# Performance work log

Measured on AMD Instinct MI355X. Metric: run time of the kernel, lower is better.

## Reference

```python
import jax, jax.numpy as jnp
import numpy as np

D_MODEL = 1024
NHEAD = 16
SPARSITY = 0.9  # keep prob = 1 - sparsity
NEG = -1e30    # stand-in for -inf; avoids NaN on (rare) fully-masked rows
EPS = 1e-5


def _layernorm(x, g, b):
    mu = jnp.mean(x, axis=-1, keepdims=True)
    var = jnp.mean(jnp.square(x - mu), axis=-1, keepdims=True)
    return (x - mu) * jax.lax.rsqrt(var + EPS) * g + b


def setup_inputs() -> dict:
    key = jax.random.key(0)
    ks = jax.random.split(key, 12)
    B, S, D = 2, 2048, D_MODEL
    H = NHEAD
    s = 1.0 / np.sqrt(D)
    inp = {
        "x": jax.random.normal(ks[0], (B, S, D), jnp.float32),
        # torch: torch.rand((B,H,S,S)) > sparsity, resampled each forward
        "mask": jax.random.uniform(ks[1], (B, H, S, S), jnp.float32) > SPARSITY,
        "Wq": jax.random.normal(ks[2], (D, D), jnp.float32) * s,
        "bq": jnp.zeros((D,), jnp.float32),
        "Wk": jax.random.normal(ks[3], (D, D), jnp.float32) * s,
        "bk": jnp.zeros((D,), jnp.float32),
        "Wv": jax.random.normal(ks[4], (D, D), jnp.float32) * s,
        "bv": jnp.zeros((D,), jnp.float32),
        "Wo": jax.random.normal(ks[5], (D, D), jnp.float32) * s,
        "bo": jnp.zeros((D,), jnp.float32),
        "ln1_g": jnp.ones((D,), jnp.float32),
        "ln1_b": jnp.zeros((D,), jnp.float32),
        "ln2_g": jnp.ones((D,), jnp.float32),
        "ln2_b": jnp.zeros((D,), jnp.float32),
        "W1": jax.random.normal(ks[6], (D, 4 * D), jnp.float32) * s,
        "b1f": jnp.zeros((4 * D,), jnp.float32),
        "W2": jax.random.normal(ks[7], (4 * D, D), jnp.float32) * (1.0 / np.sqrt(4 * D)),
        "b2f": jnp.zeros((D,), jnp.float32),
    }
    return inp


def reference(x, mask, Wq, bq, Wk, bk, Wv, bv, Wo, bo,
              ln1_g, ln1_b, ln2_g, ln2_b, W1, b1f, W2, b2f):
    B, S, D = x.shape
    H = NHEAD
    dk = D // H
    # projections -> (B, H, S, dk)
    q = (x @ Wq + bq).reshape(B, S, H, dk).transpose(0, 2, 1, 3)
    k = (x @ Wk + bk).reshape(B, S, H, dk).transpose(0, 2, 1, 3)
    v = (x @ Wv + bv).reshape(B, S, H, dk).transpose(0, 2, 1, 3)
    scores = jnp.einsum('bhqd,bhkd->bhqk', q, k) / np.sqrt(dk)
    scores = jnp.where(mask, scores, NEG)
    attn = jax.nn.softmax(scores, axis=-1)
    ctx = jnp.einsum('bhqk,bhkd->bhqd', attn, v)          # (B,H,S,dk)
    ctx = ctx.transpose(0, 2, 1, 3).reshape(B, S, D)
    attn_out = ctx @ Wo + bo
    x = _layernorm(x + attn_out, ln1_g, ln1_b)
    ff = jax.nn.relu(x @ W1 + b1f) @ W2 + b2f             # eval: dropout off
    return _layernorm(x + ff, ln2_g, ln2_b)
```

## Files before the change

kernel.cpp:

```cpp
#include <hip/hip_runtime.h>
#include <stdint.h>


typedef __attribute__((ext_vector_type(8))) short short8;
typedef __attribute__((ext_vector_type(4))) float f32x4;
typedef __attribute__((ext_vector_type(4))) unsigned short u16x4;

__device__ __forceinline__ unsigned short f2bf(float f) {
    union { float f; unsigned u; } v; v.f = f;
    unsigned r = v.u + 0x7fffu + ((v.u >> 16) & 1u);
    return (unsigned short)(r >> 16);
}

__device__ __forceinline__ void gload16(const void* gsrc, void* ldst) {
    __builtin_amdgcn_global_load_lds(
        (const __attribute__((address_space(1))) void*)gsrc,
        (__attribute__((address_space(3))) void*)ldst,
        16, 0, 0);
}

__device__ __forceinline__ int SWZ(int b) { return b ^ (((b >> 9) & 1) << 5); }

__global__ __launch_bounds__(256) void f32_to_bf16_k(
    const float* __restrict__ in, unsigned short* __restrict__ out, int n4)
{
    int i = blockIdx.x * 256 + threadIdx.x;
    if (i < n4) {
        f32x4 v = *(const f32x4*)&in[(size_t)i * 4];
        u16x4 o = { f2bf(v[0]), f2bf(v[1]), f2bf(v[2]), f2bf(v[3]) };
        *(u16x4*)&out[(size_t)i * 4] = o;
    }
}

__global__ __launch_bounds__(256) void transpose_k(
    const float* __restrict__ W, unsigned short* __restrict__ Wt, int K, int N)
{
    __shared__ float tile[32][33];
    const int n0 = blockIdx.x * 32, k0 = blockIdx.y * 32;
    const int tx = threadIdx.x & 31, ty = threadIdx.x >> 5;
#pragma unroll
    for (int i = 0; i < 32; i += 8)
        tile[ty + i][tx] = W[(size_t)(k0 + ty + i) * N + n0 + tx];
    __syncthreads();
#pragma unroll
    for (int i = 0; i < 32; i += 8)
        Wt[(size_t)(n0 + ty + i) * K + k0 + tx] = f2bf(tile[tx][ty + i]);
}

__global__ __launch_bounds__(256) void vtrans_k(
    const unsigned short* __restrict__ qkv, unsigned short* __restrict__ vt)
{
    __shared__ unsigned short tile[32][34];
    const int s0 = blockIdx.x * 32;
    const int d0 = blockIdx.y * 32;
    const int bh = blockIdx.z, b = bh >> 4, h = bh & 15;
    const int tx = threadIdx.x & 31, ty = threadIdx.x >> 5;
#pragma unroll
    for (int i = 0; i < 32; i += 8)
        tile[ty + i][tx] = qkv[(size_t)(b * 2048 + s0 + ty + i) * 3072 + 2048 + h * 64 + d0 + tx];
    __syncthreads();
#pragma unroll
    for (int i = 0; i < 32; i += 8)
        vt[((size_t)bh * 64 + d0 + ty + i) * 2048 + s0 + tx] = tile[tx][ty + i];
}

__global__ void concat3_k(const float* a, const float* b, const float* c, float* out)
{
    int i = blockIdx.x * 256 + threadIdx.x;
    if (i < 3072) out[i] = (i < 1024) ? a[i] : (i < 2048 ? b[i - 1024] : c[i - 2048]);
}

__global__ __launch_bounds__(1024) void detect_mask_k(
    const unsigned int* __restrict__ m, int* __restrict__ flag)
{
    __shared__ int f1, f2;
    if (threadIdx.x == 0) { f1 = 0; f2 = 0; }
    __syncthreads();
    int l1 = 0, l2 = 0;
    for (int i = threadIdx.x; i < 65536; i += 1024) {
        unsigned v = m[i];
        l1 |= (v > 1u);
        l2 |= (v != 0u && v != 0x3f800000u);
    }
    if (l1) atomicOr(&f1, 1);
    if (l2) atomicOr(&f2, 1);
    __syncthreads();
    if (threadIdx.x == 0) {
        int mode = 0;
        if (f1) mode = f2 ? 1 : 2;
        *flag = mode;
    }
}

__global__ __launch_bounds__(256) void pack_mask_k(
    const void* __restrict__ mask, const int* __restrict__ flag,
    unsigned long long* __restrict__ packed, long long nelem)
{
    const int mode = *flag;
    const long long stride = (long long)gridDim.x * 256;
    long long i = (long long)blockIdx.x * 256 + threadIdx.x;
    if (mode == 0) {
        const int* m = (const int*)mask;
        for (; i < nelem; i += stride) {
            unsigned long long bl = __ballot(m[i] != 0);
            if ((threadIdx.x & 63) == 0) packed[i >> 6] = bl;
        }
    } else if (mode == 1) {
        const unsigned char* m = (const unsigned char*)mask;
        for (; i < nelem; i += stride) {
            unsigned long long bl = __ballot(m[i] != 0);
            if ((threadIdx.x & 63) == 0) packed[i >> 6] = bl;
        }
    } else {
        const float* m = (const float*)mask;
        for (; i < nelem; i += stride) {
            unsigned long long bl = __ballot(m[i] != 0.f);
            if ((threadIdx.x & 63) == 0) packed[i >> 6] = bl;
        }
    }
}

template<int EPI>
__global__ __launch_bounds__(512) void gemm256_bt(
    const unsigned short* __restrict__ A, const unsigned short* __restrict__ Bt,
    const float* __restrict__ bias, void* __restrict__ Cout,
    int M, int N, int K)
{
    __shared__ __align__(16) unsigned short lds[2][2][256 * 64];
    const int t = threadIdx.x;
    const int lane = t & 63;
    const int wid = t >> 6;
    const int l16 = lane & 15, g = lane >> 4;
    const int wr = wid >> 2, wc = wid & 3;

    const int nbx = gridDim.x, nwg = nbx * gridDim.y;
    const int orig = blockIdx.y * nbx + blockIdx.x;
    const int qq = nwg >> 3, rr = nwg & 7;
    const int xcd = orig & 7, idx = orig >> 3;
    const int wg = (xcd < rr) ? (xcd * (qq + 1) + idx)
                              : (rr * (qq + 1) + (xcd - rr) * qq + idx);
    const int bm = (wg / nbx) * 256, bn = (wg % nbx) * 256;

    const int ntiles = K >> 6;
    auto kof = [&](int s) { return (s < ntiles ? s : ntiles - 1) << 6; };

    auto stage_half = [&](const unsigned short* __restrict__ P, int grow0, int k0,
                          int buf, int ab, int half) {
#pragma unroll
        for (int rnd = 0; rnd < 2; ++rnd) {
            const int off = rnd * 8192 + t * 16;
            const int sw  = SWZ(off);
            const int row = off >> 7;
            const int col = (sw & 127) >> 1;
            gload16(&P[(size_t)(grow0 + half * 128 + row) * K + k0 + col],
                    &lds[buf][ab][half * 8192 + (off >> 1)]);
        }
    };

    auto lda = [&](int buf, int m, int kc) -> short8 {
        const int byte = ((m * 32 + wr * 16 + l16) * 64 + kc * 32 + g * 8) * 2;
        return *(const short8*)((const char*)&lds[buf][0][0] + SWZ(byte));
    };
    auto ldb = [&](int buf, int n, int kc) -> short8 {
        const int byte = ((n * 64 + wc * 16 + l16) * 64 + kc * 32 + g * 8) * 2;
        return *(const short8*)((const char*)&lds[buf][1][0] + SWZ(byte));
    };

    f32x4 acc[8][4] = {};
    short8 af[4][2];

    stage_half(A,  bm, 0,  0, 0, 0);
    stage_half(A,  bm, 0,  0, 0, 1);
    stage_half(Bt, bn, 0,  0, 1, 0);
    stage_half(Bt, bn, 0,  0, 1, 1);
    stage_half(A,  bm, 64, 1, 0, 0);
    stage_half(Bt, bn, 64, 1, 1, 0);
    asm volatile("s_waitcnt vmcnt(4)" ::: "memory");
    __builtin_amdgcn_s_barrier();

#define PH(buf, mh, nh, doLoadA, STAGE_STMT, doVM)                                  \
  {                                                                                  \
    if (doLoadA) {                                                                   \
      _Pragma("unroll") for (int mm = 0; mm < 4; ++mm)                               \
      _Pragma("unroll") for (int kc = 0; kc < 2; ++kc)                               \
        af[mm][kc] = lda(buf, (mh) * 4 + mm, kc);                                    \
    }                                                                                \
    short8 bf[2][2];                                                                 \
    _Pragma("unroll") for (int nn = 0; nn < 2; ++nn)                                 \
    _Pragma("unroll") for (int kc = 0; kc < 2; ++kc)                                 \
      bf[nn][kc] = ldb(buf, (nh) * 2 + nn, kc);                                      \
    STAGE_STMT;                                                                      \
    __builtin_amdgcn_s_barrier();                                                    \
    __builtin_amdgcn_s_setprio(1);                                                   \
    _Pragma("unroll") for (int mm = 0; mm < 4; ++mm)                                 \
    _Pragma("unroll") for (int nn = 0; nn < 2; ++nn)                                 \
    _Pragma("unroll") for (int kc = 0; kc < 2; ++kc)                                 \
      acc[(mh) * 4 + mm][(nh) * 2 + nn] = __builtin_amdgcn_mfma_f32_16x16x32_bf16(   \
          af[mm][kc], bf[nn][kc], acc[(mh) * 4 + mm][(nh) * 2 + nn], 0, 0, 0);       \
    __builtin_amdgcn_s_setprio(0);                                                   \
    if (doVM) { asm volatile("s_waitcnt vmcnt(4)" ::: "memory"); }                   \
    __builtin_amdgcn_s_barrier();                                                    \
  }

    const int half_ntiles = ntiles >> 1;
    for (int i = 0; i < half_ntiles; ++i) {
        const int k1 = (2 * i + 1) << 6;
        const int k2 = kof(2 * i + 2);
        const int k3 = kof(2 * i + 3);
        PH(0, 0, 0, 1, (stage_half(A,  bm, k1, 1, 0, 1)), 0)
        PH(0, 0, 1, 0, (stage_half(Bt, bn, k1, 1, 1, 1)), 0)
        PH(0, 1, 0, 1, (stage_half(A,  bm, k2, 0, 0, 0)), 0)
        PH(0, 1, 1, 0, (stage_half(Bt, bn, k2, 0, 1, 0)), 1)
        PH(1, 0, 0, 1, (stage_half(A,  bm, k2, 0, 0, 1)), 0)
        PH(1, 0, 1, 0, (stage_half(Bt, bn, k2, 0, 1, 1)), 0)
        PH(1, 1, 0, 1, (stage_half(A,  bm, k3, 1, 0, 0)), 0)
        PH(1, 1, 1, 0, (stage_half(Bt, bn, k3, 1, 1, 0)), 1)
    }
#undef PH

#pragma unroll
    for (int m = 0; m < 8; ++m) {
        const int row0 = bm + m * 32 + wr * 16 + g * 4;
#pragma unroll
        for (int n = 0; n < 4; ++n) {
            const int col = bn + n * 64 + wc * 16 + l16;
            const float bb = bias[col];
#pragma unroll
            for (int r = 0; r < 4; ++r) {
                float v = acc[m][n][r] + bb;
                if (EPI == 1) v = fmaxf(v, 0.f);
                ((unsigned short*)Cout)[(size_t)(row0 + r) * N + col] = f2bf(v);
            }
        }
    }
}

template<int EPI>
__global__ __launch_bounds__(256) void gemm_bt(
    const unsigned short* __restrict__ A, const unsigned short* __restrict__ Bt,
    const float* __restrict__ bias, const float* __restrict__ resid,
    void* __restrict__ Cout, int M, int N, int K)
{
    __shared__ unsigned short As[128 * 64];
    __shared__ unsigned short Bs[128 * 64];
    const int t = threadIdx.x;
    const int lane = t & 63, wid = t >> 6;
    const int l16 = lane & 15, g = lane >> 4;
    const int wr = wid >> 1, wc = wid & 1;
    const int bm = blockIdx.y * 128, bn = blockIdx.x * 128;

    f32x4 acc[4][4] = {};

    for (int k0 = 0; k0 < K; k0 += 64) {
        __syncthreads();
#pragma unroll
        for (int i = 0; i < 4; ++i) {
            int linear = i * 2048 + t * 8;
            int row = linear >> 6, col = linear & 63;
            gload16(&A[(size_t)(bm + row) * K + k0 + col], &As[linear]);
        }
#pragma unroll
        for (int i = 0; i < 4; ++i) {
            int linear = i * 2048 + t * 8;
            int row = linear >> 6, col = linear & 63;
            gload16(&Bt[(size_t)(bn + row) * K + k0 + col], &Bs[linear]);
        }
        __syncthreads();
#pragma unroll
        for (int kc = 0; kc < 2; ++kc) {
            short8 a[4], b[4];
#pragma unroll
            for (int m = 0; m < 4; ++m)
                a[m] = *(const short8*)&As[(wr * 64 + m * 16 + l16) * 64 + kc * 32 + g * 8];
#pragma unroll
            for (int n = 0; n < 4; ++n)
                b[n] = *(const short8*)&Bs[(wc * 64 + n * 16 + l16) * 64 + kc * 32 + g * 8];
#pragma unroll
            for (int m = 0; m < 4; ++m)
#pragma unroll
                for (int n = 0; n < 4; ++n)
                    acc[m][n] = __builtin_amdgcn_mfma_f32_16x16x32_bf16(a[m], b[n], acc[m][n], 0, 0, 0);
        }
    }

#pragma unroll
    for (int m = 0; m < 4; ++m) {
        const int row0 = bm + wr * 64 + m * 16 + g * 4;
#pragma unroll
        for (int n = 0; n < 4; ++n) {
            const int col = bn + wc * 64 + n * 16 + l16;
            const float bb = bias[col];
#pragma unroll
            for (int r = 0; r < 4; ++r) {
                float v = acc[m][n][r] + bb;
                const size_t idx = (size_t)(row0 + r) * N + col;
                if (EPI == 2) {
                    ((float*)Cout)[idx] = v + resid[idx];
                } else {
                    if (EPI == 1) v = fmaxf(v, 0.f);
                    ((unsigned short*)Cout)[idx] = f2bf(v);
                }
            }
        }
    }
}

__global__ __launch_bounds__(256) void attn_k(
    const unsigned short* __restrict__ qkv,
    const unsigned short* __restrict__ vt,
    const unsigned long long* __restrict__ pmask,
    unsigned short* __restrict__ ctx)
{
    __shared__ unsigned short Pl[4][16 * 72];
    const int t = threadIdx.x, lane = t & 63, w = t >> 6;
    const int l16 = lane & 15, g = lane >> 4;
    const int bh = blockIdx.y;
    const int b = bh >> 4, h = bh & 15;
    const int q0 = blockIdx.x * 64;

    const size_t rowQ = (size_t)(b * 2048 + q0 + w * 16 + l16) * 3072 + h * 64;
    const short8 qf0 = *(const short8*)&qkv[rowQ + g * 8];
    const short8 qf1 = *(const short8*)&qkv[rowQ + 32 + g * 8];

    const unsigned long long* mbase =
        pmask + ((size_t)bh * 2048 + q0 + w * 16 + g * 4) * 32;
    const unsigned short* vbase = &vt[(size_t)bh * 64 * 2048];

    f32x4 acc[4] = {};
    float lrow[4] = { 0.f, 0.f, 0.f, 0.f };

    for (int kt = 0; kt < 32; ++kt) {
        unsigned long long mw[4];
#pragma unroll
        for (int j = 0; j < 4; ++j) mw[j] = mbase[j * 32 + kt];

        f32x4 s[4] = {};
        __builtin_amdgcn_s_setprio(1);
#pragma unroll
        for (int n = 0; n < 4; ++n) {
            const size_t rowK = (size_t)(b * 2048 + kt * 64 + n * 16 + l16) * 3072 + 1024 + h * 64;
            const short8 kf0 = *(const short8*)&qkv[rowK + g * 8];
            const short8 kf1 = *(const short8*)&qkv[rowK + 32 + g * 8];
            s[n] = __builtin_amdgcn_mfma_f32_16x16x32_bf16(qf0, kf0, s[n], 0, 0, 0);
            s[n] = __builtin_amdgcn_mfma_f32_16x16x32_bf16(qf1, kf1, s[n], 0, 0, 0);
        }
        __builtin_amdgcn_s_setprio(0);

#pragma unroll
        for (int n = 0; n < 4; ++n) {
            const int sh = n * 16 + l16;
#pragma unroll
            for (int j = 0; j < 4; ++j) {
                const bool keep = (mw[j] >> sh) & 1ull;
                const float p = keep ? __expf(s[n][j] * 0.125f) : 0.f;
                s[n][j] = p;
                lrow[j] += p;
            }
        }

#pragma unroll
        for (int n = 0; n < 4; ++n)
#pragma unroll
            for (int j = 0; j < 4; ++j)
                Pl[w][(g * 4 + j) * 72 + n * 16 + l16] = f2bf(s[n][j]);

        __builtin_amdgcn_s_setprio(1);
#pragma unroll
        for (int c = 0; c < 2; ++c) {
            const short8 pf = *(const short8*)&Pl[w][l16 * 72 + c * 32 + g * 8];
#pragma unroll
            for (int n = 0; n < 4; ++n) {
                const short8 vf = *(const short8*)&vbase[(size_t)(n * 16 + l16) * 2048 + kt * 64 + c * 32 + g * 8];
                acc[n] = __builtin_amdgcn_mfma_f32_16x16x32_bf16(pf, vf, acc[n], 0, 0, 0);
            }
        }
        __builtin_amdgcn_s_setprio(0);
    }

#pragma unroll
    for (int j = 0; j < 4; ++j) {
#pragma unroll
        for (int d = 1; d < 16; d <<= 1) lrow[j] += __shfl_xor(lrow[j], d);
        lrow[j] = 1.f / fmaxf(lrow[j], 1e-30f);
    }

#pragma unroll
    for (int n = 0; n < 4; ++n)
#pragma unroll
        for (int j = 0; j < 4; ++j) {
            const int q = q0 + w * 16 + g * 4 + j;
            ctx[(size_t)(b * 2048 + q) * 1024 + h * 64 + n * 16 + l16] = f2bf(acc[n][j] * lrow[j]);
        }
}

template<int WB>
__global__ __launch_bounds__(256) void ln_k(
    const float* __restrict__ in, const float* __restrict__ gw, const float* __restrict__ bw,
    float* __restrict__ outF, unsigned short* __restrict__ outB)
{
    __shared__ float red[2][4];
    const int row = blockIdx.x, t = threadIdx.x;
    const f32x4 v = *(const f32x4*)&in[(size_t)row * 1024 + t * 4];
    float s = v[0] + v[1] + v[2] + v[3];
    float ss = v[0] * v[0] + v[1] * v[1] + v[2] * v[2] + v[3] * v[3];
#pragma unroll
    for (int d = 1; d < 64; d <<= 1) { s += __shfl_xor(s, d); ss += __shfl_xor(ss, d); }
    if ((t & 63) == 0) { red[0][t >> 6] = s; red[1][t >> 6] = ss; }
    __syncthreads();
    s = red[0][0] + red[0][1] + red[0][2] + red[0][3];
    ss = red[1][0] + red[1][1] + red[1][2] + red[1][3];
    const float mu = s * (1.f / 1024.f);
    const float var = ss * (1.f / 1024.f) - mu * mu;
    const float rs = rsqrtf(var + 1e-5f);
    f32x4 y;
#pragma unroll
    for (int e = 0; e < 4; ++e)
        y[e] = (v[e] - mu) * rs * gw[t * 4 + e] + bw[t * 4 + e];
    *(f32x4*)&outF[(size_t)row * 1024 + t * 4] = y;
    if (WB) {
        u16x4 o = { f2bf(y[0]), f2bf(y[1]), f2bf(y[2]), f2bf(y[3]) };
        *(u16x4*)&outB[(size_t)row * 1024 + t * 4] = o;
    }
}

extern "C" void kernel_launch(void* const* d_in, const int* in_sizes, int n_in,
                              void* d_out, int out_size, void* d_ws, size_t ws_size,
                              hipStream_t stream)
{
    (void)n_in; (void)out_size; (void)ws_size;
    const float* x   = (const float*)d_in[0];
    const void*  mask = d_in[1];
    const float* Wq  = (const float*)d_in[2];
    const float* bq  = (const float*)d_in[3];
    const float* Wk  = (const float*)d_in[4];
    const float* bk  = (const float*)d_in[5];
    const float* Wv  = (const float*)d_in[6];
    const float* bv  = (const float*)d_in[7];
    const float* Wo  = (const float*)d_in[8];
    const float* bo  = (const float*)d_in[9];
    const float* g1  = (const float*)d_in[10];
    const float* be1 = (const float*)d_in[11];
    const float* g2  = (const float*)d_in[12];
    const float* be2 = (const float*)d_in[13];
    const float* W1  = (const float*)d_in[14];
    const float* b1  = (const float*)d_in[15];
    const float* W2  = (const float*)d_in[16];
    const float* b2  = (const float*)d_in[17];

    const int M = 4096;
    const long long maskN = in_sizes[1];

    char* wsb = (char*)d_ws;
    size_t off = 0;
    auto alloc = [&](size_t bytes) -> char* {
        char* p = wsb + off;
        off += (bytes + 255) & ~(size_t)255;
        return p;
    };
    int*            flag   = (int*)           alloc(256);
    unsigned long long* pm = (unsigned long long*)alloc((size_t)(maskN / 64) * 8);
    unsigned short* xb     = (unsigned short*)alloc((size_t)M * 1024 * 2);
    unsigned short* wqkvT  = (unsigned short*)alloc((size_t)3072 * 1024 * 2);
    unsigned short* woT    = (unsigned short*)alloc((size_t)1024 * 1024 * 2);
    unsigned short* w1T    = (unsigned short*)alloc((size_t)4096 * 1024 * 2);
    unsigned short* w2T    = (unsigned short*)alloc((size_t)1024 * 4096 * 2);
    float*          bqkv   = (float*)         alloc(3072 * 4);
    unsigned short* qkv    = (unsigned short*)alloc((size_t)M * 3072 * 2);
    unsigned short* vtb    = (unsigned short*)alloc((size_t)32 * 64 * 2048 * 2);
    unsigned short* ctxb   = (unsigned short*)alloc((size_t)M * 1024 * 2);
    float*          r1f    = (float*)         alloc((size_t)M * 1024 * 4);
    float*          x1f    = (float*)         alloc((size_t)M * 1024 * 4);
    unsigned short* x1b    = (unsigned short*)alloc((size_t)M * 1024 * 2);
    unsigned short* hb     = (unsigned short*)alloc((size_t)M * 4096 * 2);

    detect_mask_k<<<1, 1024, 0, stream>>>((const unsigned int*)mask, flag);
    pack_mask_k<<<2048, 256, 0, stream>>>(mask, flag, pm, maskN);
    f32_to_bf16_k<<<4096, 256, 0, stream>>>(x, xb, M * 1024 / 4);
    transpose_k<<<dim3(32, 32),  256, 0, stream>>>(Wq, wqkvT,                1024, 1024);
    transpose_k<<<dim3(32, 32),  256, 0, stream>>>(Wk, wqkvT + 1024 * 1024,  1024, 1024);
    transpose_k<<<dim3(32, 32),  256, 0, stream>>>(Wv, wqkvT + 2048 * 1024,  1024, 1024);
    transpose_k<<<dim3(32, 32),  256, 0, stream>>>(Wo, woT,                  1024, 1024);
    transpose_k<<<dim3(128, 32), 256, 0, stream>>>(W1, w1T, 1024, 4096);
    transpose_k<<<dim3(32, 128), 256, 0, stream>>>(W2, w2T, 4096, 1024);
    concat3_k<<<12, 256, 0, stream>>>(bq, bk, bv, bqkv);

    gemm256_bt<0><<<dim3(12, 16), 512, 0, stream>>>(xb, wqkvT, bqkv, qkv, M, 3072, 1024);
    vtrans_k<<<dim3(64, 2, 32), 256, 0, stream>>>(qkv, vtb);
    attn_k<<<dim3(32, 32), 256, 0, stream>>>(qkv, vtb, pm, ctxb);
    gemm_bt<2><<<dim3(8, 32), 256, 0, stream>>>(ctxb, woT, bo, x, r1f, M, 1024, 1024);
    ln_k<1><<<4096, 256, 0, stream>>>(r1f, g1, be1, x1f, x1b);
    gemm256_bt<1><<<dim3(16, 16), 512, 0, stream>>>(x1b, w1T, b1, hb, M, 4096, 1024);
    gemm_bt<2><<<dim3(8, 32), 256, 0, stream>>>(hb, w2T, b2, x1f, r1f, M, 1024, 4096);
    ln_k<0><<<4096, 256, 0, stream>>>(r1f, g2, be2, (float*)d_out, nullptr);
}
```

Baseline: 1.286 ms.

## Stage K/V tiles in double-buffered swizzled LDS and enlarge attention blocks

The attention kernel now loads each 64-key K tile and V^T tile into LDS with async global-to-LDS loads. It double-buffers them so the next tile's load overlaps the current compute, and uses an XOR swizzle to avoid bank conflicts. Blocks grow to 512 threads covering 128 queries, so each staged tile is shared by 8 waves instead of each wave reading K/V from global memory itself. The mask-detection scan also reads a quarter as many words. This adds two barriers per iteration, uses more LDS, and halves the number of attention blocks.

```diff
diff --git a/kernel.cpp b/kernel.cpp
--- a/kernel.cpp
+++ b/kernel.cpp
@@ -77,7 +77,7 @@
     if (threadIdx.x == 0) { f1 = 0; f2 = 0; }
     __syncthreads();
     int l1 = 0, l2 = 0;
-    for (int i = threadIdx.x; i < 65536; i += 1024) {
+    for (int i = threadIdx.x; i < 16384; i += 1024) {
         unsigned v = m[i];
         l1 |= (v > 1u);
         l2 |= (v != 0u && v != 0x3f800000u);
@@ -305,18 +305,20 @@
     }
 }
 
-__global__ __launch_bounds__(256) void attn_k(
+__global__ __launch_bounds__(512) void attn_k(
     const unsigned short* __restrict__ qkv,
     const unsigned short* __restrict__ vt,
     const unsigned long long* __restrict__ pmask,
     unsigned short* __restrict__ ctx)
 {
-    __shared__ unsigned short Pl[4][16 * 72];
+    __shared__ __align__(16) unsigned short Ks[2][64 * 64];
+    __shared__ __align__(16) unsigned short Vs[2][64 * 64];
+    __shared__ unsigned short Pl[8][16 * 72];
     const int t = threadIdx.x, lane = t & 63, w = t >> 6;
     const int l16 = lane & 15, g = lane >> 4;
     const int bh = blockIdx.y;
     const int b = bh >> 4, h = bh & 15;
-    const int q0 = blockIdx.x * 64;
+    const int q0 = blockIdx.x * 128;
 
     const size_t rowQ = (size_t)(b * 2048 + q0 + w * 16 + l16) * 3072 + h * 64;
     const short8 qf0 = *(const short8*)&qkv[rowQ + g * 8];
@@ -324,12 +326,45 @@
 
     const unsigned long long* mbase =
         pmask + ((size_t)bh * 2048 + q0 + w * 16 + g * 4) * 32;
+
+    const int soff = t * 16;
+    const int srow = soff >> 7;
+    const int scol = ((soff & 127) ^ ((srow & 7) << 4)) >> 1;
+    const size_t kRowBase = (size_t)(b * 2048) * 3072 + 1024 + h * 64;
     const unsigned short* vbase = &vt[(size_t)bh * 64 * 2048];
+
+    auto stageK = [&](int buf, int kt) {
+        gload16(&qkv[kRowBase + (size_t)(kt * 64 + srow) * 3072 + scol],
+                &Ks[buf][soff >> 1]);
+    };
+    auto stageV = [&](int buf, int kt) {
+        gload16(&vbase[(size_t)srow * 2048 + kt * 64 + scol],
+                &Vs[buf][soff >> 1]);
+    };
+    auto ldK = [&](int buf, int r, int kc) -> short8 {
+        const int byte = r * 128 + ((kc * 64 + g * 16) ^ ((r & 7) << 4));
+        return *(const short8*)((const char*)Ks[buf] + byte);
+    };
+    auto ldV = [&](int buf, int r, int kc) -> short8 {
+        const int byte = r * 128 + ((kc * 64 + g * 16) ^ ((r & 7) << 4));
+        return *(const short8*)((const char*)Vs[buf] + byte);
+    };
 
     f32x4 acc[4] = {};
     float lrow[4] = { 0.f, 0.f, 0.f, 0.f };
 
+    stageK(0, 0);
+    stageV(0, 0);
+
+    int buf = 0;
     for (int kt = 0; kt < 32; ++kt) {
+        const int knext = (kt < 31) ? kt + 1 : 31;
+        stageK(buf ^ 1, knext);
+        stageV(buf ^ 1, knext);
+        asm volatile("s_waitcnt vmcnt(2)" ::: "memory");
+        __builtin_amdgcn_s_barrier();
+        asm volatile("" ::: "memory");
+
         unsigned long long mw[4];
 #pragma unroll
         for (int j = 0; j < 4; ++j) mw[j] = mbase[j * 32 + kt];
@@ -338,9 +373,8 @@
         __builtin_amdgcn_s_setprio(1);
 #pragma unroll
         for (int n = 0; n < 4; ++n) {
-            const size_t rowK = (size_t)(b * 2048 + kt * 64 + n * 16 + l16) * 3072 + 1024 + h * 64;
-            const short8 kf0 = *(const short8*)&qkv[rowK + g * 8];
-            const short8 kf1 = *(const short8*)&qkv[rowK + 32 + g * 8];
+            const short8 kf0 = ldK(buf, n * 16 + l16, 0);
+            const short8 kf1 = ldK(buf, n * 16 + l16, 1);
             s[n] = __builtin_amdgcn_mfma_f32_16x16x32_bf16(qf0, kf0, s[n], 0, 0, 0);
             s[n] = __builtin_amdgcn_mfma_f32_16x16x32_bf16(qf1, kf1, s[n], 0, 0, 0);
         }
@@ -370,11 +404,15 @@
             const short8 pf = *(const short8*)&Pl[w][l16 * 72 + c * 32 + g * 8];
 #pragma unroll
             for (int n = 0; n < 4; ++n) {
-                const short8 vf = *(const short8*)&vbase[(size_t)(n * 16 + l16) * 2048 + kt * 64 + c * 32 + g * 8];
+                const short8 vf = ldV(buf, n * 16 + l16, c);
                 acc[n] = __builtin_amdgcn_mfma_f32_16x16x32_bf16(pf, vf, acc[n], 0, 0, 0);
             }
         }
         __builtin_amdgcn_s_setprio(0);
+
+        asm volatile("" ::: "memory");
+        __builtin_amdgcn_s_barrier();
+        buf ^= 1;
     }
 
 #pragma unroll
@@ -486,7 +524,7 @@
 
     gemm256_bt<0><<<dim3(12, 16), 512, 0, stream>>>(xb, wqkvT, bqkv, qkv, M, 3072, 1024);
     vtrans_k<<<dim3(64, 2, 32), 256, 0, stream>>>(qkv, vtb);
-    attn_k<<<dim3(32, 32), 256, 0, stream>>>(qkv, vtb, pm, ctxb);
+    attn_k<<<dim3(16, 32), 512, 0, stream>>>(qkv, vtb, pm, ctxb);
     gemm_bt<2><<<dim3(8, 32), 256, 0, stream>>>(ctxb, woT, bo, x, r1f, M, 1024, 1024);
     ln_k<1><<<4096, 256, 0, stream>>>(r1f, g1, be1, x1f, x1b);
     gemm256_bt<1><<<dim3(16, 16), 512, 0, stream>>>(x1b, w1T, b1, hb, M, 4096, 1024);
```

New measurement: 1.110 ms. 1.16x faster.
